# Kernel tuning notes

Hardware: AMD Instinct MI355X
Metric: run time of the kernel (lower is better)

The kernel has to match this reference:

```python
import jax, jax.numpy as jnp
import numpy as np

N, F_IN, H, MH = 50000, 128, 128, 256
E = 800000

def _lin_init(key, out_d, in_d, bias=True):
    k1, k2 = jax.random.split(key)
    bound = 1.0 / np.sqrt(in_d)
    W = jax.random.uniform(k1, (out_d, in_d), minval=-bound, maxval=bound, dtype=jnp.float32)
    if bias:
        b = jax.random.uniform(k2, (out_d,), minval=-bound, maxval=bound, dtype=jnp.float32)
        return W, b
    return W, None

def setup_inputs() -> dict:
    key = jax.random.key(0)
    ks = jax.random.split(key, 8)
    x = jax.random.normal(ks[0], (N, F_IN), dtype=jnp.float32)
    edge_index = jax.random.randint(ks[1], (2, E), 0, N, dtype=jnp.int64)
    W1l, b1l = _lin_init(ks[2], H, F_IN, bias=True)   # SAGEConv1 neighbor lin (with bias)
    W1r, _ = _lin_init(ks[3], H, F_IN, bias=False)    # SAGEConv1 root lin (no bias)
    W2l, b2l = _lin_init(ks[4], H, H, bias=True)
    W2r, _ = _lin_init(ks[5], H, H, bias=False)
    Wm1, bm1 = _lin_init(ks[6], MH, 2 * H, bias=True)
    Wm2, bm2 = _lin_init(ks[7], 1, MH, bias=True)
    return {"x": x, "edge_index": edge_index,
            "W1l": W1l, "b1l": b1l, "W1r": W1r,
            "W2l": W2l, "b2l": b2l, "W2r": W2r,
            "Wm1": Wm1, "bm1": bm1, "Wm2": Wm2, "bm2": bm2}

def _sage_conv(x, src, dst, Wl, bl, Wr, num_nodes):
    # mean-aggregate messages x[src] at dst, then lin_l(agg) + lin_r(x)
    agg = jax.ops.segment_sum(x[src], dst, num_segments=num_nodes)
    cnt = jax.ops.segment_sum(jnp.ones((src.shape[0],), x.dtype), dst, num_segments=num_nodes)
    agg = agg / jnp.maximum(cnt, 1.0)[:, None]
    return agg @ Wl.T + bl + x @ Wr.T

def reference(x, edge_index, W1l, b1l, W1r, W2l, b2l, W2r, Wm1, bm1, Wm2, bm2):
    src, dst = edge_index[0], edge_index[1]
    n = x.shape[0]
    h = jax.nn.relu(_sage_conv(x, src, dst, W1l, b1l, W1r, n))
    # dropout is identity in eval mode
    h = jax.nn.relu(_sage_conv(h, src, dst, W2l, b2l, W2r, n))
    ef = jnp.concatenate([h[src], h[dst]], axis=-1)  # [E, 2H]
    out = jax.nn.relu(ef @ Wm1.T + bm1) @ Wm2.T + bm2
    return out.reshape(-1)
```

## Files before the change

kernel.cpp:

```cpp
#include <hip/hip_runtime.h>
#include <hip/hip_bf16.h>

#define NN 50000
#define F 128
#define EE 800000
#define MHD 256

typedef __attribute__((ext_vector_type(8))) short bf16x8;
typedef __attribute__((ext_vector_type(4))) float f32x4;

__device__ __forceinline__ float b2f(unsigned short u) {
    union { unsigned int i; float f; } v; v.i = ((unsigned)u) << 16; return v.f;
}
__device__ __forceinline__ unsigned short f2b(float f) {
    unsigned int x = __float_as_uint(f);
    unsigned int r = x + 0x7fffu + ((x >> 16) & 1u);
    return (unsigned short)(r >> 16);
}

__global__ __launch_bounds__(256) void cast_zero_kernel(
    const float* __restrict__ x,
    const float* __restrict__ W1l, const float* __restrict__ W1r,
    const float* __restrict__ W2l, const float* __restrict__ W2r,
    const float* __restrict__ Wm1,
    unsigned short* __restrict__ xb, unsigned short* __restrict__ wb,
    int* __restrict__ deg) {
    int bid = blockIdx.x;
    if (bid < 6250) {
        int i = (bid * 256 + threadIdx.x) * 4;
        float4 v = *(const float4*)(x + i);
        ushort4 o; o.x = f2b(v.x); o.y = f2b(v.y); o.z = f2b(v.z); o.w = f2b(v.w);
        *(ushort4*)(xb + i) = o;
    } else if (bid < 6378) {
        int i = ((bid - 6250) * 256 + threadIdx.x) * 4;
        unsigned short o[4];
        if (i < 32768) {
            const float* p = (i < 16384) ? (W1l + i) : (W1r + (i - 16384));
            float4 v = *(const float4*)p;
            o[0] = f2b(v.x); o[1] = f2b(v.y); o[2] = f2b(v.z); o[3] = f2b(v.w);
        } else if (i < 65536) {
            int local = i - 32768;
            const float* M = (local < 16384) ? W2l : W2r;
            int lm = local & 16383;
            int n = lm >> 7, kp = lm & 127;
#pragma unroll
            for (int t = 0; t < 4; t++) {
                int k = ((kp + t) & 7) * 16 + ((kp + t) >> 3);
                o[t] = f2b(M[n * 128 + k]);
            }
        } else {
            int local = i - 65536;
            int n = local >> 8, k2 = local & 255;
            int half = k2 >> 7, kp = k2 & 127;
#pragma unroll
            for (int t = 0; t < 4; t++) {
                int k = half * 128 + ((kp + t) & 7) * 16 + ((kp + t) >> 3);
                o[t] = f2b(Wm1[n * 256 + k]);
            }
        }
        *(ushort4*)(wb + i) = *(ushort4*)o;
    } else {
        int idx = ((bid - 6378) * 256 + threadIdx.x) * 4;
        if (idx < 50016) *(int4*)(deg + idx) = (int4){0, 0, 0, 0};
    }
}

__global__ __launch_bounds__(256) void edge_cvt_hist_kernel(
    const int* __restrict__ ei, int* __restrict__ s32, int* __restrict__ d32,
    int* __restrict__ deg) {
    __shared__ int isI64;
    if (threadIdx.x == 0) {
        int z = 0;
        for (int i = 1; i < 128; i += 2) z |= ei[i];
        isI64 = (z == 0) ? 1 : 0;
    }
    __syncthreads();
    int e = blockIdx.x * 256 + threadIdx.x;
    if (e >= EE) return;
    int s, d;
    if (isI64) {
        const long long* e64 = (const long long*)ei;
        s = (int)e64[e];
        d = (int)e64[EE + e];
    } else {
        s = ei[e];
        d = ei[EE + e];
    }
    s32[e] = s;
    d32[e] = d;
    atomicAdd(&deg[d], 1);
}

__global__ __launch_bounds__(1024) void scan_p1_kernel(
    const int* __restrict__ deg, int* __restrict__ exloc, int* __restrict__ bsum) {
    __shared__ int part[1024];
    int t = threadIdx.x, gid = blockIdx.x * 1024 + t;
    int v = (gid < NN) ? deg[gid] : 0;
    part[t] = v;
    __syncthreads();
    for (int off = 1; off < 1024; off <<= 1) {
        int u = (t >= off) ? part[t - off] : 0;
        __syncthreads();
        part[t] += u;
        __syncthreads();
    }
    exloc[gid] = part[t] - v;
    if (t == 1023) bsum[blockIdx.x] = part[t];
}

__global__ __launch_bounds__(1024) void scan_p3_kernel(
    const int* __restrict__ exloc, const int* __restrict__ bsum,
    int* __restrict__ rowstart, int* __restrict__ cursor) {
    __shared__ int offs;
    if (threadIdx.x == 0) {
        int s = 0;
        for (int b = 0; b < blockIdx.x; b++) s += bsum[b];
        offs = s;
    }
    __syncthreads();
    int gid = blockIdx.x * 1024 + threadIdx.x;
    if (gid > NN) return;
    if (gid == NN) { rowstart[NN] = EE; return; }
    int r = exloc[gid] + offs;
    rowstart[gid] = r;
    cursor[gid] = r;
}

__global__ __launch_bounds__(256) void fill_kernel(
    const int* __restrict__ s32, const int* __restrict__ d32,
    int* __restrict__ cursor, int2* __restrict__ nedge) {
    int e = blockIdx.x * 256 + threadIdx.x;
    if (e < EE) {
        int p = atomicAdd(&cursor[d32[e]], 1);
        nedge[p] = make_int2(s32[e], e);
    }
}

__global__ __launch_bounds__(256) void sage_layer_kernel(
    const unsigned short* __restrict__ xin,
    const int2* __restrict__ nedge, const int* __restrict__ rowstart,
    const unsigned short* __restrict__ W1, const unsigned short* __restrict__ W2,
    const float* __restrict__ bias,
    unsigned short* __restrict__ out) {
    __shared__ unsigned short lds[4][16][136];
    int wave = threadIdx.x >> 6, lane = threadIdx.x & 63;
    int m0 = (blockIdx.x * 4 + wave) * 16;

    int g = lane >> 4, l16 = lane & 15, col8 = l16 * 8;
    for (int batch = 0; batch < 4; batch++) {
        int node = m0 + batch * 4 + g;
        int beg = 0, end = 0;
        if (node < NN) { beg = rowstart[node]; end = rowstart[node + 1]; }
        float a[8] = {0,0,0,0,0,0,0,0};
        float b[8] = {0,0,0,0,0,0,0,0};
        int j = beg;
        for (; j + 7 < end; j += 8) {
            int s0 = nedge[j].x,     s1 = nedge[j + 1].x, s2 = nedge[j + 2].x, s3 = nedge[j + 3].x;
            int s4 = nedge[j + 4].x, s5 = nedge[j + 5].x, s6 = nedge[j + 6].x, s7 = nedge[j + 7].x;
            bf16x8 v0 = *(const bf16x8*)(xin + (size_t)s0 * F + col8);
            bf16x8 v1 = *(const bf16x8*)(xin + (size_t)s1 * F + col8);
            bf16x8 v2 = *(const bf16x8*)(xin + (size_t)s2 * F + col8);
            bf16x8 v3 = *(const bf16x8*)(xin + (size_t)s3 * F + col8);
            bf16x8 v4 = *(const bf16x8*)(xin + (size_t)s4 * F + col8);
            bf16x8 v5 = *(const bf16x8*)(xin + (size_t)s5 * F + col8);
            bf16x8 v6 = *(const bf16x8*)(xin + (size_t)s6 * F + col8);
            bf16x8 v7 = *(const bf16x8*)(xin + (size_t)s7 * F + col8);
            for (int i = 0; i < 8; i++)
                a[i] += (b2f((unsigned short)v0[i]) + b2f((unsigned short)v1[i]))
                      + (b2f((unsigned short)v2[i]) + b2f((unsigned short)v3[i]));
            for (int i = 0; i < 8; i++)
                b[i] += (b2f((unsigned short)v4[i]) + b2f((unsigned short)v5[i]))
                      + (b2f((unsigned short)v6[i]) + b2f((unsigned short)v7[i]));
        }
        for (; j + 3 < end; j += 4) {
            int s0 = nedge[j].x, s1 = nedge[j + 1].x, s2 = nedge[j + 2].x, s3 = nedge[j + 3].x;
            bf16x8 v0 = *(const bf16x8*)(xin + (size_t)s0 * F + col8);
            bf16x8 v1 = *(const bf16x8*)(xin + (size_t)s1 * F + col8);
            bf16x8 v2 = *(const bf16x8*)(xin + (size_t)s2 * F + col8);
            bf16x8 v3 = *(const bf16x8*)(xin + (size_t)s3 * F + col8);
            for (int i = 0; i < 8; i++)
                a[i] += (b2f((unsigned short)v0[i]) + b2f((unsigned short)v1[i]))
                      + (b2f((unsigned short)v2[i]) + b2f((unsigned short)v3[i]));
        }
        for (; j < end; j++) {
            int s0 = nedge[j].x;
            bf16x8 v0 = *(const bf16x8*)(xin + (size_t)s0 * F + col8);
            for (int i = 0; i < 8; i++) a[i] += b2f((unsigned short)v0[i]);
        }
        float inv = 1.0f / fmaxf((float)(end - beg), 1.0f);
        unsigned short o[8];
        for (int i = 0; i < 8; i++) o[i] = f2b((a[i] + b[i]) * inv);
        *(bf16x8*)&lds[wave][batch * 4 + g][col8] = *(bf16x8*)o;
    }
    __syncthreads();

    int c = lane & 15, q = lane >> 4;
    f32x4 acc[8];
    for (int nt = 0; nt < 8; nt++) {
        float b = bias[nt * 16 + c];
        acc[nt] = (f32x4){b, b, b, b};
    }
    int mrow = m0 + c; if (mrow > NN - 1) mrow = NN - 1;
    for (int op = 0; op < 2; op++) {
        const unsigned short* W = op ? W2 : W1;
        for (int kb = 0; kb < 4; kb++) {
            bf16x8 a;
            if (op == 0) a = *(const bf16x8*)&lds[wave][c][kb * 32 + q * 8];
            else         a = *(const bf16x8*)(xin + (size_t)mrow * F + kb * 32 + q * 8);
            for (int nt = 0; nt < 8; nt++) {
                bf16x8 b = *(const bf16x8*)(W + (size_t)(nt * 16 + c) * F + kb * 32 + q * 8);
                acc[nt] = __builtin_amdgcn_mfma_f32_16x16x32_bf16(a, b, acc[nt], 0, 0, 0);
            }
        }
    }
#pragma unroll
    for (int r = 0; r < 4; r++) {
        int node = m0 + q * 4 + r;
        if (node < NN) {
            unsigned short o[8];
#pragma unroll
            for (int nt = 0; nt < 8; nt++) o[nt] = f2b(fmaxf(acc[nt][r], 0.0f));
            *(bf16x8*)(out + (size_t)node * F + c * 8) = *(bf16x8*)o;
        }
    }
}

__global__ __launch_bounds__(256) void pq_gemm_kernel(
    const unsigned short* __restrict__ h,
    const unsigned short* __restrict__ wmb,
    const float* __restrict__ bm1,
    unsigned short* __restrict__ PQ) {
    int wave = threadIdx.x >> 6, lane = threadIdx.x & 63;
    int c = lane & 15, q = lane >> 4;
    int half = wave >> 1, ntBase = (wave & 1) * 8;
    int m0 = blockIdx.x * 16;
    int mrow = m0 + c; if (mrow > NN - 1) mrow = NN - 1;
    bf16x8 a[4];
#pragma unroll
    for (int kb = 0; kb < 4; kb++)
        a[kb] = *(const bf16x8*)(h + (size_t)mrow * F + kb * 32 + q * 8);
    f32x4 acc[8];
#pragma unroll
    for (int nt = 0; nt < 8; nt++) {
        float b = half ? bm1[(ntBase + nt) * 16 + c] : 0.0f;
        acc[nt] = (f32x4){b, b, b, b};
    }
#pragma unroll
    for (int kb = 0; kb < 4; kb++) {
#pragma unroll
        for (int nt = 0; nt < 8; nt++) {
            bf16x8 b = *(const bf16x8*)(wmb + (size_t)((ntBase + nt) * 16 + c) * 256 + half * 128 + kb * 32 + q * 8);
            acc[nt] = __builtin_amdgcn_mfma_f32_16x16x32_bf16(a[kb], b, acc[nt], 0, 0, 0);
        }
    }
#pragma unroll
    for (int r = 0; r < 4; r++) {
        int node = m0 + q * 4 + r;
        if (node < NN) {
            unsigned short o[8];
#pragma unroll
            for (int nt = 0; nt < 8; nt++) o[nt] = f2b(acc[nt][r]);
            *(bf16x8*)(PQ + (size_t)node * 512 + half * 256 + c * 16 + ntBase) = *(bf16x8*)o;
        }
    }
}

__global__ __launch_bounds__(256) void edge_dot_kernel(
    const unsigned short* __restrict__ PQ,
    const int2* __restrict__ nedge, const int* __restrict__ rowstart,
    const float* __restrict__ Wm2, const float* __restrict__ bm2,
    float* __restrict__ out) {
    int wave = threadIdx.x >> 6, lane = threadIdx.x & 63;
    int node = blockIdx.x * 4 + wave;
    if (node >= NN) return;
    int g = lane >> 4, l16 = lane & 15;
    int col = l16 * 16;
    float w2f[16], qf[16];
#pragma unroll
    for (int i = 0; i < 16; i++) w2f[i] = Wm2[i * 16 + l16];
    {
        bf16x8 q0 = *(const bf16x8*)(PQ + (size_t)node * 512 + 256 + col);
        bf16x8 q1 = *(const bf16x8*)(PQ + (size_t)node * 512 + 256 + col + 8);
#pragma unroll
        for (int i = 0; i < 8; i++) { qf[i] = b2f((unsigned short)q0[i]); qf[8 + i] = b2f((unsigned short)q1[i]); }
    }
    float b2 = bm2[0];
    int beg = rowstart[node], end = rowstart[node + 1];
    int j = beg + g;
    for (; j + 4 < end; j += 8) {
        int2 e0 = nedge[j], e1 = nedge[j + 4];
        uint4 a0 = *(const uint4*)(PQ + (size_t)e0.x * 512 + col);
        uint4 a1 = *(const uint4*)(PQ + (size_t)e0.x * 512 + col + 8);
        uint4 c0 = *(const uint4*)(PQ + (size_t)e1.x * 512 + col);
        uint4 c1 = *(const uint4*)(PQ + (size_t)e1.x * 512 + col + 8);
        float t0 = 0.f, t1 = 0.f;
        unsigned int w0[8] = {a0.x, a0.y, a0.z, a0.w, a1.x, a1.y, a1.z, a1.w};
        unsigned int w1[8] = {c0.x, c0.y, c0.z, c0.w, c1.x, c1.y, c1.z, c1.w};
#pragma unroll
        for (int i = 0; i < 8; i++) {
            float lo0 = __uint_as_float(w0[i] << 16);
            float hi0 = __uint_as_float(w0[i] & 0xffff0000u);
            float lo1 = __uint_as_float(w1[i] << 16);
            float hi1 = __uint_as_float(w1[i] & 0xffff0000u);
            t0 += fmaxf(lo0 + qf[2 * i], 0.f) * w2f[2 * i]
                + fmaxf(hi0 + qf[2 * i + 1], 0.f) * w2f[2 * i + 1];
            t1 += fmaxf(lo1 + qf[2 * i], 0.f) * w2f[2 * i]
                + fmaxf(hi1 + qf[2 * i + 1], 0.f) * w2f[2 * i + 1];
        }
        t0 += __shfl_xor(t0, 1);  t1 += __shfl_xor(t1, 1);
        t0 += __shfl_xor(t0, 2);  t1 += __shfl_xor(t1, 2);
        t0 += __shfl_xor(t0, 4);  t1 += __shfl_xor(t1, 4);
        t0 += __shfl_xor(t0, 8);  t1 += __shfl_xor(t1, 8);
        if (l16 == 0) { out[e0.y] = t0 + b2; out[e1.y] = t1 + b2; }
    }
    for (; j < end; j += 4) {
        int2 e0 = nedge[j];
        uint4 a0 = *(const uint4*)(PQ + (size_t)e0.x * 512 + col);
        uint4 a1 = *(const uint4*)(PQ + (size_t)e0.x * 512 + col + 8);
        unsigned int w0[8] = {a0.x, a0.y, a0.z, a0.w, a1.x, a1.y, a1.z, a1.w};
        float t = 0.f;
#pragma unroll
        for (int i = 0; i < 8; i++) {
            float lo = __uint_as_float(w0[i] << 16);
            float hi = __uint_as_float(w0[i] & 0xffff0000u);
            t += fmaxf(lo + qf[2 * i], 0.f) * w2f[2 * i]
               + fmaxf(hi + qf[2 * i + 1], 0.f) * w2f[2 * i + 1];
        }
        t += __shfl_xor(t, 1);
        t += __shfl_xor(t, 2);
        t += __shfl_xor(t, 4);
        t += __shfl_xor(t, 8);
        if (l16 == 0) out[e0.y] = t + b2;
    }
}

extern "C" void kernel_launch(void* const* d_in, const int* in_sizes, int n_in,
                              void* d_out, int out_size, void* d_ws, size_t ws_size,
                              hipStream_t stream) {
    const float* x   = (const float*)d_in[0];
    const int*   ei  = (const int*)d_in[1];
    const float* W1l = (const float*)d_in[2];
    const float* b1l = (const float*)d_in[3];
    const float* W1r = (const float*)d_in[4];
    const float* W2l = (const float*)d_in[5];
    const float* b2l = (const float*)d_in[6];
    const float* W2r = (const float*)d_in[7];
    const float* Wm1 = (const float*)d_in[8];
    const float* bm1 = (const float*)d_in[9];
    const float* Wm2 = (const float*)d_in[10];
    const float* bm2 = (const float*)d_in[11];

    char* ws = (char*)d_ws;
    unsigned short* PQ       = (unsigned short*)(ws);
    unsigned short* xb       = (unsigned short*)(ws);
    unsigned short* h1       = (unsigned short*)(ws + 12800000);
    unsigned short* wb       = (unsigned short*)(ws + 51200000);
    int*            s32      = (int*)(ws + 51462144);
    int*            d32      = (int*)(ws + 54662144);
    int*            deg      = (int*)(ws + 57862144);
    int*            rowstart = (int*)(ws + 58062208);
    int*            cursor   = (int*)(ws + 58262272);
    int2*           nedge    = (int2*)(ws + 58462336);
    unsigned short* h2       = (unsigned short*)(ws + 64862336);
    int*            exloc    = (int*)(ws + 77662336);
    int*            bsum     = (int*)(ws + 77867136);
    float*          outp     = (float*)d_out;

    const unsigned short* w1l_b  = wb;
    const unsigned short* w1r_b  = wb + 16384;
    const unsigned short* w2l_p  = wb + 32768;
    const unsigned short* w2r_p  = wb + 49152;
    const unsigned short* wm1_p  = wb + 65536;

    cast_zero_kernel<<<6427, 256, 0, stream>>>(x, W1l, W1r, W2l, W2r, Wm1, xb, wb, deg);
    edge_cvt_hist_kernel<<<3125, 256, 0, stream>>>(ei, s32, d32, deg);
    scan_p1_kernel<<<50, 1024, 0, stream>>>(deg, exloc, bsum);
    scan_p3_kernel<<<50, 1024, 0, stream>>>(exloc, bsum, rowstart, cursor);
    fill_kernel<<<3125, 256, 0, stream>>>(s32, d32, cursor, nedge);

    sage_layer_kernel<<<782, 256, 0, stream>>>(xb, nedge, rowstart, w1l_b, w1r_b, b1l, h1);
    sage_layer_kernel<<<782, 256, 0, stream>>>(h1, nedge, rowstart, w2l_p, w2r_p, b2l, h2);
    pq_gemm_kernel<<<3125, 256, 0, stream>>>(h2, wm1_p, bm1, PQ);
    edge_dot_kernel<<<12500, 256, 0, stream>>>(PQ, nedge, rowstart, Wm2, bm2, outp);
}
```

Measured before the change: 424.5 us.

## Fuse PQ GEMM into second SAGE layer and drop int32 edge staging

```diff
diff --git a/kernel.cpp b/kernel.cpp
--- a/kernel.cpp
+++ b/kernel.cpp
@@ -65,9 +65,58 @@
     }
 }
 
-__global__ __launch_bounds__(256) void edge_cvt_hist_kernel(
-    const int* __restrict__ ei, int* __restrict__ s32, int* __restrict__ d32,
-    int* __restrict__ deg) {
+__global__ __launch_bounds__(256) void hist_kernel(
+    const int* __restrict__ ei, int* __restrict__ deg) {
+    __shared__ int isI64;
+    if (threadIdx.x == 0) {
+        int z = 0;
+        for (int i = 1; i < 128; i += 2) z |= ei[i];
+        isI64 = (z == 0) ? 1 : 0;
+    }
+    __syncthreads();
+    int e = blockIdx.x * 256 + threadIdx.x;
+    if (e >= EE) return;
+    int d = isI64 ? (int)((const long long*)ei)[EE + e] : ei[EE + e];
+    atomicAdd(&deg[d], 1);
+}
+
+__global__ __launch_bounds__(1024) void scan_p1_kernel(
+    const int* __restrict__ deg, int* __restrict__ exloc, int* __restrict__ bsum) {
+    __shared__ int part[1024];
+    int t = threadIdx.x, gid = blockIdx.x * 1024 + t;
+    int v = (gid < NN) ? deg[gid] : 0;
+    part[t] = v;
+    __syncthreads();
+    for (int off = 1; off < 1024; off <<= 1) {
+        int u = (t >= off) ? part[t - off] : 0;
+        __syncthreads();
+        part[t] += u;
+        __syncthreads();
+    }
+    exloc[gid] = part[t] - v;
+    if (t == 1023) bsum[blockIdx.x] = part[t];
+}
+
+__global__ __launch_bounds__(1024) void scan_p3_kernel(
+    const int* __restrict__ exloc, const int* __restrict__ bsum,
+    int* __restrict__ rowstart, int* __restrict__ cursor) {
+    __shared__ int offs;
+    if (threadIdx.x == 0) {
+        int s = 0;
+        for (int b = 0; b < blockIdx.x; b++) s += bsum[b];
+        offs = s;
+    }
+    __syncthreads();
+    int gid = blockIdx.x * 1024 + threadIdx.x;
+    if (gid > NN) return;
+    if (gid == NN) { rowstart[NN] = EE; return; }
+    int r = exloc[gid] + offs;
+    rowstart[gid] = r;
+    cursor[gid] = r;
+}
+
+__global__ __launch_bounds__(256) void fill_kernel(
+    const int* __restrict__ ei, int* __restrict__ cursor, int2* __restrict__ nedge) {
     __shared__ int isI64;
     if (threadIdx.x == 0) {
         int z = 0;
@@ -86,54 +135,8 @@
         s = ei[e];
         d = ei[EE + e];
     }
-    s32[e] = s;
-    d32[e] = d;
-    atomicAdd(&deg[d], 1);
-}
-
-__global__ __launch_bounds__(1024) void scan_p1_kernel(
-    const int* __restrict__ deg, int* __restrict__ exloc, int* __restrict__ bsum) {
-    __shared__ int part[1024];
-    int t = threadIdx.x, gid = blockIdx.x * 1024 + t;
-    int v = (gid < NN) ? deg[gid] : 0;
-    part[t] = v;
-    __syncthreads();
-    for (int off = 1; off < 1024; off <<= 1) {
-        int u = (t >= off) ? part[t - off] : 0;
-        __syncthreads();
-        part[t] += u;
-        __syncthreads();
-    }
-    exloc[gid] = part[t] - v;
-    if (t == 1023) bsum[blockIdx.x] = part[t];
-}
-
-__global__ __launch_bounds__(1024) void scan_p3_kernel(
-    const int* __restrict__ exloc, const int* __restrict__ bsum,
-    int* __restrict__ rowstart, int* __restrict__ cursor) {
-    __shared__ int offs;
-    if (threadIdx.x == 0) {
-        int s = 0;
-        for (int b = 0; b < blockIdx.x; b++) s += bsum[b];
-        offs = s;
-    }
-    __syncthreads();
-    int gid = blockIdx.x * 1024 + threadIdx.x;
-    if (gid > NN) return;
-    if (gid == NN) { rowstart[NN] = EE; return; }
-    int r = exloc[gid] + offs;
-    rowstart[gid] = r;
-    cursor[gid] = r;
-}
-
-__global__ __launch_bounds__(256) void fill_kernel(
-    const int* __restrict__ s32, const int* __restrict__ d32,
-    int* __restrict__ cursor, int2* __restrict__ nedge) {
-    int e = blockIdx.x * 256 + threadIdx.x;
-    if (e < EE) {
-        int p = atomicAdd(&cursor[d32[e]], 1);
-        nedge[p] = make_int2(s32[e], e);
-    }
+    int p = atomicAdd(&cursor[d], 1);
+    nedge[p] = make_int2(s, e);
 }
 
 __global__ __launch_bounds__(256) void sage_layer_kernel(
@@ -141,7 +144,11 @@
     const int2* __restrict__ nedge, const int* __restrict__ rowstart,
     const unsigned short* __restrict__ W1, const unsigned short* __restrict__ W2,
     const float* __restrict__ bias,
-    unsigned short* __restrict__ out) {
+    unsigned short* __restrict__ hout,
+    const unsigned short* __restrict__ wmb,
+    const float* __restrict__ bm1,
+    unsigned short* __restrict__ PQ,
+    int doPQ) {
     __shared__ unsigned short lds[4][16][136];
     int wave = threadIdx.x >> 6, lane = threadIdx.x & 63;
     int m0 = (blockIdx.x * 4 + wave) * 16;
@@ -213,54 +220,50 @@
             }
         }
     }
+    __syncthreads();
 #pragma unroll
     for (int r = 0; r < 4; r++) {
         int node = m0 + q * 4 + r;
-        if (node < NN) {
-            unsigned short o[8];
-#pragma unroll
-            for (int nt = 0; nt < 8; nt++) o[nt] = f2b(fmaxf(acc[nt][r], 0.0f));
-            *(bf16x8*)(out + (size_t)node * F + c * 8) = *(bf16x8*)o;
-        }
-    }
-}
-
-__global__ __launch_bounds__(256) void pq_gemm_kernel(
-    const unsigned short* __restrict__ h,
-    const unsigned short* __restrict__ wmb,
-    const float* __restrict__ bm1,
-    unsigned short* __restrict__ PQ) {
-    int wave = threadIdx.x >> 6, lane = threadIdx.x & 63;
-    int c = lane & 15, q = lane >> 4;
-    int half = wave >> 1, ntBase = (wave & 1) * 8;
-    int m0 = blockIdx.x * 16;
-    int mrow = m0 + c; if (mrow > NN - 1) mrow = NN - 1;
-    bf16x8 a[4];
+        unsigned short o[8];
+#pragma unroll
+        for (int nt = 0; nt < 8; nt++) o[nt] = f2b(fmaxf(acc[nt][r], 0.0f));
+        if (hout && node < NN)
+            *(bf16x8*)(hout + (size_t)node * F + c * 8) = *(bf16x8*)o;
+        if (doPQ)
+            *(bf16x8*)&lds[wave][q * 4 + r][c * 8] = *(bf16x8*)o;
+    }
+    if (!doPQ) return;
+    __syncthreads();
+
+    bf16x8 a2[4];
 #pragma unroll
     for (int kb = 0; kb < 4; kb++)
-        a[kb] = *(const bf16x8*)(h + (size_t)mrow * F + kb * 32 + q * 8);
-    f32x4 acc[8];
-#pragma unroll
-    for (int nt = 0; nt < 8; nt++) {
-        float b = half ? bm1[(ntBase + nt) * 16 + c] : 0.0f;
-        acc[nt] = (f32x4){b, b, b, b};
-    }
-#pragma unroll
-    for (int kb = 0; kb < 4; kb++) {
+        a2[kb] = *(const bf16x8*)&lds[wave][c][kb * 32 + q * 8];
+    for (int grp = 0; grp < 4; grp++) {
+        int half = grp >> 1, ntBase = (grp & 1) * 8;
+        f32x4 pacc[8];
 #pragma unroll
         for (int nt = 0; nt < 8; nt++) {
-            bf16x8 b = *(const bf16x8*)(wmb + (size_t)((ntBase + nt) * 16 + c) * 256 + half * 128 + kb * 32 + q * 8);
-            acc[nt] = __builtin_amdgcn_mfma_f32_16x16x32_bf16(a[kb], b, acc[nt], 0, 0, 0);
-        }
-    }
-#pragma unroll
-    for (int r = 0; r < 4; r++) {
-        int node = m0 + q * 4 + r;
-        if (node < NN) {
-            unsigned short o[8];
-#pragma unroll
-            for (int nt = 0; nt < 8; nt++) o[nt] = f2b(acc[nt][r]);
-            *(bf16x8*)(PQ + (size_t)node * 512 + half * 256 + c * 16 + ntBase) = *(bf16x8*)o;
+            float b = half ? bm1[(ntBase + nt) * 16 + c] : 0.0f;
+            pacc[nt] = (f32x4){b, b, b, b};
+        }
+#pragma unroll
+        for (int kb = 0; kb < 4; kb++) {
+#pragma unroll
+            for (int nt = 0; nt < 8; nt++) {
+                bf16x8 b = *(const bf16x8*)(wmb + (size_t)((ntBase + nt) * 16 + c) * 256 + half * 128 + kb * 32 + q * 8);
+                pacc[nt] = __builtin_amdgcn_mfma_f32_16x16x32_bf16(a2[kb], b, pacc[nt], 0, 0, 0);
+            }
+        }
+#pragma unroll
+        for (int r = 0; r < 4; r++) {
+            int node = m0 + q * 4 + r;
+            if (node < NN) {
+                unsigned short o[8];
+#pragma unroll
+                for (int nt = 0; nt < 8; nt++) o[nt] = f2b(pacc[nt][r]);
+                *(bf16x8*)(PQ + (size_t)node * 512 + half * 256 + c * 16 + ntBase) = *(bf16x8*)o;
+            }
         }
     }
 }
@@ -355,16 +358,15 @@
     unsigned short* xb       = (unsigned short*)(ws);
     unsigned short* h1       = (unsigned short*)(ws + 12800000);
     unsigned short* wb       = (unsigned short*)(ws + 51200000);
-    int*            s32      = (int*)(ws + 51462144);
-    int*            d32      = (int*)(ws + 54662144);
     int*            deg      = (int*)(ws + 57862144);
     int*            rowstart = (int*)(ws + 58062208);
     int*            cursor   = (int*)(ws + 58262272);
     int2*           nedge    = (int2*)(ws + 58462336);
-    unsigned short* h2       = (unsigned short*)(ws + 64862336);
     int*            exloc    = (int*)(ws + 77662336);
     int*            bsum     = (int*)(ws + 77867136);
     float*          outp     = (float*)d_out;
+
+    PQ = (unsigned short*)(ws + 83967136);
 
     const unsigned short* w1l_b  = wb;
     const unsigned short* w1r_b  = wb + 16384;
@@ -373,13 +375,14 @@
     const unsigned short* wm1_p  = wb + 65536;
 
     cast_zero_kernel<<<6427, 256, 0, stream>>>(x, W1l, W1r, W2l, W2r, Wm1, xb, wb, deg);
-    edge_cvt_hist_kernel<<<3125, 256, 0, stream>>>(ei, s32, d32, deg);
+    hist_kernel<<<3125, 256, 0, stream>>>(ei, deg);
     scan_p1_kernel<<<50, 1024, 0, stream>>>(deg, exloc, bsum);
     scan_p3_kernel<<<50, 1024, 0, stream>>>(exloc, bsum, rowstart, cursor);
-    fill_kernel<<<3125, 256, 0, stream>>>(s32, d32, cursor, nedge);
-
-    sage_layer_kernel<<<782, 256, 0, stream>>>(xb, nedge, rowstart, w1l_b, w1r_b, b1l, h1);
-    sage_layer_kernel<<<782, 256, 0, stream>>>(h1, nedge, rowstart, w2l_p, w2r_p, b2l, h2);
-    pq_gemm_kernel<<<3125, 256, 0, stream>>>(h2, wm1_p, bm1, PQ);
+    fill_kernel<<<3125, 256, 0, stream>>>(ei, cursor, nedge);
+
+    sage_layer_kernel<<<782, 256, 0, stream>>>(xb, nedge, rowstart, w1l_b, w1r_b, b1l,
+                                               h1, nullptr, nullptr, nullptr, 0);
+    sage_layer_kernel<<<782, 256, 0, stream>>>(h1, nedge, rowstart, w2l_p, w2r_p, b2l,
+                                               nullptr, wm1_p, bm1, PQ, 1);
     edge_dot_kernel<<<12500, 256, 0, stream>>>(PQ, nedge, rowstart, Wm2, bm2, outp);
 }
```

Measured after the change: 475.7 us. 12.1% more time.
